# Optimization experiments

Hardware: AMD Instinct MI355X
Metric: run time of the kernel (lower is better)

## Reference

```python
import jax, jax.numpy as jnp
import numpy as np

HIDDEN = 4096
N_HEADS = 32
HEAD_DIM = HIDDEN // N_HEADS
B = 8
S = 1024
N = B * S


def _build_cos_sin(max_pos, head_dim):
    inv_freq = 1.0 / (10000.0 ** (np.arange(0, head_dim, 2, dtype=np.float32) / head_dim))
    t = np.arange(max_pos, dtype=np.float32)
    freqs = np.outer(t, inv_freq)                 # [max_pos, head_dim/2]
    emb = np.concatenate([freqs, freqs], axis=-1)  # [max_pos, head_dim]
    return jnp.asarray(np.cos(emb)), jnp.asarray(np.sin(emb))


def setup_inputs() -> dict:
    key = jax.random.key(0)
    ks = jax.random.split(key, 5)
    cos, sin = _build_cos_sin(S, HEAD_DIM)
    scale = 0.02
    inp = {
        "cos": cos,
        "sin": sin,
        "nz_hidden_states": jax.random.normal(ks[0], (N, HIDDEN), jnp.float32),
        "nz_position_ids": jnp.tile(jnp.arange(S, dtype=jnp.int32), B),
        "cu_seqlens": jnp.arange(B + 1, dtype=jnp.int32) * S,
        "max_seqlen": S,
        "Wq": jax.random.normal(ks[1], (HIDDEN, HIDDEN), jnp.float32) * scale,
        "Wk": jax.random.normal(ks[2], (HIDDEN, HIDDEN), jnp.float32) * scale,
        "Wv": jax.random.normal(ks[3], (HIDDEN, HIDDEN), jnp.float32) * scale,
        "Wo": jax.random.normal(ks[4], (HIDDEN, HIDDEN), jnp.float32) * scale,
    }
    return inp


def _rotate_half(x):
    x1, x2 = jnp.split(x, 2, axis=-1)
    return jnp.concatenate([-x2, x1], axis=-1)


def reference(cos, sin, nz_hidden_states, nz_position_ids, cu_seqlens, max_seqlen, Wq, Wk, Wv, Wo):
    n_tok = nz_hidden_states.shape[0]
    b = cu_seqlens.shape[0] - 1
    s = n_tok // b  # equal-length packing
    h, d = N_HEADS, HEAD_DIM

    q = (nz_hidden_states @ Wq.T).reshape(n_tok, h, d)
    k = (nz_hidden_states @ Wk.T).reshape(n_tok, h, d)
    v = (nz_hidden_states @ Wv.T).reshape(n_tok, h, d)

    # RoPE: cos/sin gathered per token, broadcast over heads
    c = cos[nz_position_ids][:, None, :]  # [N,1,D]
    sn = sin[nz_position_ids][:, None, :]
    q = q * c + _rotate_half(q) * sn
    k = k * c + _rotate_half(k) * sn

    # Varlen causal attention (equal-length segments -> batch reshape)
    qb = q.reshape(b, s, h, d)
    kb = k.reshape(b, s, h, d)
    vb = v.reshape(b, s, h, d)
    scores = jnp.einsum('bqhd,bkhd->bhqk', qb, kb) / jnp.sqrt(jnp.float32(d))
    causal = jnp.tril(jnp.ones((s, s), dtype=bool))
    scores = jnp.where(causal, scores, jnp.finfo(scores.dtype).min)
    probs = jax.nn.softmax(scores, axis=-1)
    out = jnp.einsum('bhqk,bkhd->bqhd', probs, vb).reshape(n_tok, h * d)
    return out @ Wo.T
```

## Files before the change

kernel.cpp:

```cpp
#include <hip/hip_runtime.h>
#include <hip/hip_bf16.h>

#define NTOK 8192
#define HID 4096
#define NHEADS 32
#define HDIM 128
#define SEQ 1024
#define NSTEP (HID / 32)

typedef float f32x4 __attribute__((ext_vector_type(4)));
typedef short bf16x8 __attribute__((ext_vector_type(8)));

__device__ __forceinline__ ushort f2bf(float f) {
  union { float f; unsigned u; } x;
  x.f = f;
  unsigned r = x.u + 0x7fffu + ((x.u >> 16) & 1u);
  return (ushort)(r >> 16);
}
__device__ __forceinline__ float bf2f(ushort h) {
  union { unsigned u; float f; } x;
  x.u = ((unsigned)h) << 16;
  return x.f;
}

__global__ __launch_bounds__(256) void cvt_bf16_kernel(const float4* __restrict__ in,
                                                       ushort4* __restrict__ out, int n4) {
  int i = blockIdx.x * 256 + threadIdx.x;
  if (i < n4) {
    float4 v = in[i];
    ushort4 o;
    o.x = f2bf(v.x); o.y = f2bf(v.y); o.z = f2bf(v.z); o.w = f2bf(v.w);
    out[i] = o;
  }
}


__device__ __forceinline__ void gload16(const void* g, void* l) {
  __builtin_amdgcn_global_load_lds(
      (const __attribute__((address_space(1))) unsigned int*)g,
      (__attribute__((address_space(3))) unsigned int*)l, 16, 0, 0);
}

__device__ __forceinline__ void stage32(const ushort* gA, const ushort* gB,
                                        int rowA0, int rowB0, int k0,
                                        ushort* ldsA, ushort* ldsB, int tid) {
  const int wid = tid >> 6, lane = tid & 63;
#pragma unroll
  for (int q = 0; q < 2; ++q) {
    int wuni = q * 8192 + wid * 1024;
    int off = wuni + lane * 16;
    int row = off >> 6;
    int kb = (off ^ (((row >> 1) & 3) << 4)) & 63;
    gload16(gA + (size_t)(rowA0 + row) * HID + k0 + (kb >> 1), (char*)ldsA + wuni);
    gload16(gB + (size_t)(rowB0 + row) * HID + k0 + (kb >> 1), (char*)ldsB + wuni);
  }
}

#define GSTEP(T, DO_STAGE, VMC)                                                \
  do {                                                                         \
    const char* cA = (const char*)ringA[(T) & 3];                              \
    const char* cB = (const char*)ringB[(T) & 3];                              \
    _Pragma("unroll") for (int ii = 0; ii < 8; ++ii) {                         \
      int L = (wm * 128 + ii * 16 + l15) * 64 + l4 * 16;                       \
      af[ii] = *(const bf16x8*)(cA + (L ^ swzr));                              \
    }                                                                          \
    _Pragma("unroll") for (int jj = 0; jj < 4; ++jj) {                         \
      int L = (wn * 64 + jj * 16 + l15) * 64 + l4 * 16;                        \
      bfr[jj] = *(const bf16x8*)(cB + (L ^ swzr));                             \
    }                                                                          \
    if (DO_STAGE)                                                              \
      stage32(Abf, Bp, m0, n0, ((T) + 3) * 32, ringA[((T) + 3) & 3],           \
              ringB[((T) + 3) & 3], tid);                                      \
    _Pragma("unroll") for (int ii = 0; ii < 8; ++ii)                           \
        _Pragma("unroll") for (int jj = 0; jj < 4; ++jj)                       \
            acc[ii][jj] = __builtin_amdgcn_mfma_f32_16x16x32_bf16(             \
                af[ii], bfr[jj], acc[ii][jj], 0, 0, 0);                        \
    if ((VMC) >= 0) {                                                          \
      asm volatile("s_waitcnt lgkmcnt(0)" ::: "memory");                       \
      if ((VMC) == 4) asm volatile("s_waitcnt vmcnt(4)" ::: "memory");         \
      else asm volatile("s_waitcnt vmcnt(0)" ::: "memory");                    \
      __builtin_amdgcn_s_barrier();                                            \
    }                                                                          \
  } while (0)

template <bool OUTF32>
__global__ __launch_bounds__(512, 2) void gemm256_kernel(
    const ushort* __restrict__ Abf,
    const ushort* __restrict__ B0, const ushort* __restrict__ B1,
    const ushort* __restrict__ B2,
    void* __restrict__ O0, void* __restrict__ O1, void* __restrict__ O2,
    int NTALL) {
  __shared__ __align__(16) ushort ringA[4][8192];
  __shared__ __align__(16) ushort ringB[4][8192];

  const int tid = threadIdx.x;
  const int l = tid & 63, wid = tid >> 6;
  const int wm = wid >> 2, wn = wid & 3;
  const int l15 = l & 15, l4 = l >> 4;
  const int swzr = ((l15 >> 1) & 3) << 4;

  const int nwg = gridDim.x;
  const int cpx = nwg >> 3;
  const int bid = blockIdx.x;
  const int lgid = (bid & 7) * cpx + (bid >> 3);
  const int bandw = NTALL << 3;
  const int band = lgid / bandw, rem = lgid % bandw;
  const int nt = rem >> 3;
  const int mt = (band << 3) + (rem & 7);
  const int m0 = mt * 256;
  const int sel = nt >> 4;
  const int n0 = (nt & 15) * 256;
  const ushort* Bp = (sel == 0) ? B0 : ((sel == 1) ? B1 : B2);
  void* Op = (sel == 0) ? O0 : ((sel == 1) ? O1 : O2);

  f32x4 acc[8][4];
  const f32x4 zero = {0.f, 0.f, 0.f, 0.f};
#pragma unroll
  for (int i = 0; i < 8; ++i)
#pragma unroll
    for (int j = 0; j < 4; ++j) acc[i][j] = zero;

  stage32(Abf, Bp, m0, n0, 0, ringA[0], ringB[0], tid);
  stage32(Abf, Bp, m0, n0, 32, ringA[1], ringB[1], tid);
  stage32(Abf, Bp, m0, n0, 64, ringA[2], ringB[2], tid);
  asm volatile("s_waitcnt vmcnt(4)" ::: "memory");
  __builtin_amdgcn_s_barrier();

  bf16x8 af[8], bfr[4];
  for (int tt = 0; tt < NSTEP - 4; tt += 4) {
    GSTEP(tt + 0, true, 4);
    GSTEP(tt + 1, true, 4);
    GSTEP(tt + 2, true, 4);
    GSTEP(tt + 3, true, 4);
  }
  GSTEP(NSTEP - 4, true, 4);
  GSTEP(NSTEP - 3, false, 0);
  GSTEP(NSTEP - 2, false, -1);
  GSTEP(NSTEP - 1, false, -1);

#pragma unroll
  for (int i = 0; i < 8; ++i) {
    const int row = m0 + wm * 128 + i * 16 + l4 * 4;
#pragma unroll
    for (int j = 0; j < 4; ++j) {
      const int col = n0 + wn * 64 + j * 16 + l15;
#pragma unroll
      for (int r = 0; r < 4; ++r) {
        float v = acc[i][j][r];
        if constexpr (OUTF32)
          ((float*)Op)[(size_t)(row + r) * HID + col] = v;
        else
          ((ushort*)Op)[(size_t)(row + r) * HID + col] = f2bf(v);
      }
    }
  }
}

template <bool ISBF>
__device__ __forceinline__ void stage_tile(ushort* lds, const void* gp, int row0, int k0, int tid) {
  if constexpr (ISBF) {
    const ushort* g = (const ushort*)gp;
#pragma unroll
    for (int i = 0; i < 2; ++i) {
      int row = (tid >> 2) + i * 64;
      int gr = tid & 3;
      bf16x8 v = *(const bf16x8*)(g + (size_t)(row0 + row) * HID + k0 + gr * 8);
      int gs = gr ^ ((row >> 1) & 3);
      *(bf16x8*)((char*)lds + row * 64 + gs * 16) = v;
    }
  } else {
    const float* g = (const float*)gp;
    int row = tid >> 1;
    const float* rp = g + (size_t)(row0 + row) * HID + k0;
#pragma unroll
    for (int i = 0; i < 2; ++i) {
      int gr = (tid & 1) * 2 + i;
      float4 a = *(const float4*)(rp + gr * 8);
      float4 b = *(const float4*)(rp + gr * 8 + 4);
      bf16x8 v;
      v[0] = (short)f2bf(a.x); v[1] = (short)f2bf(a.y);
      v[2] = (short)f2bf(a.z); v[3] = (short)f2bf(a.w);
      v[4] = (short)f2bf(b.x); v[5] = (short)f2bf(b.y);
      v[6] = (short)f2bf(b.z); v[7] = (short)f2bf(b.w);
      int gs = gr ^ ((row >> 1) & 3);
      *(bf16x8*)((char*)lds + row * 64 + gs * 16) = v;
    }
  }
}

template <bool ABF, bool BBF, bool OUTF32>
__global__ __launch_bounds__(256) void gemm_bt_kernel(
    const void* __restrict__ Ap,
    const void* __restrict__ B0, const void* __restrict__ B1, const void* __restrict__ B2,
    void* __restrict__ O0, void* __restrict__ O1, void* __restrict__ O2,
    int ntiles_per_w) {
  __shared__ __align__(16) ushort lA[128 * 32];
  __shared__ __align__(16) ushort lB[128 * 32];
  const int tid = threadIdx.x;
  const int l = tid & 63, wid = tid >> 6;
  const int wm = wid >> 1, wn = wid & 1;
  const int l15 = l & 15, l4 = l >> 4;
  const int mt0 = blockIdx.y * 128;
  const int ntile = blockIdx.x;
  const int sel = ntile / ntiles_per_w;
  const int nt0 = (ntile % ntiles_per_w) * 128;
  const void* Bp = (sel == 0) ? B0 : ((sel == 1) ? B1 : B2);
  void* Op = (sel == 0) ? O0 : ((sel == 1) ? O1 : O2);

  const f32x4 zero = {0.f, 0.f, 0.f, 0.f};
  f32x4 acc[4][4];
#pragma unroll
  for (int i = 0; i < 4; ++i)
#pragma unroll
    for (int j = 0; j < 4; ++j) acc[i][j] = zero;

  for (int k0 = 0; k0 < HID; k0 += 32) {
    stage_tile<ABF>(lA, Ap, mt0, k0, tid);
    stage_tile<BBF>(lB, Bp, nt0, k0, tid);
    __syncthreads();
    bf16x8 af[4], bfr[4];
#pragma unroll
    for (int i = 0; i < 4; ++i) {
      int rowa = wm * 64 + i * 16 + l15;
      int ga = l4 ^ ((rowa >> 1) & 3);
      af[i] = *(const bf16x8*)((const char*)lA + rowa * 64 + ga * 16);
      int rowb = wn * 64 + i * 16 + l15;
      int gb = l4 ^ ((rowb >> 1) & 3);
      bfr[i] = *(const bf16x8*)((const char*)lB + rowb * 64 + gb * 16);
    }
#pragma unroll
    for (int i = 0; i < 4; ++i)
#pragma unroll
      for (int j = 0; j < 4; ++j)
        acc[i][j] = __builtin_amdgcn_mfma_f32_16x16x32_bf16(af[i], bfr[j], acc[i][j], 0, 0, 0);
    __syncthreads();
  }

#pragma unroll
  for (int i = 0; i < 4; ++i) {
#pragma unroll
    for (int j = 0; j < 4; ++j) {
      int row = mt0 + wm * 64 + i * 16 + l4 * 4;
      int col = nt0 + wn * 64 + j * 16 + l15;
#pragma unroll
      for (int r = 0; r < 4; ++r) {
        float v = acc[i][j][r];
        if constexpr (OUTF32)
          ((float*)Op)[(size_t)(row + r) * HID + col] = v;
        else
          ((ushort*)Op)[(size_t)(row + r) * HID + col] = f2bf(v);
      }
    }
  }
}

__global__ __launch_bounds__(256) void rope_kernel(
    ushort* __restrict__ q, ushort* __restrict__ k,
    const float* __restrict__ cosT, const float* __restrict__ sinT,
    const int* __restrict__ pos) {
  int idx = blockIdx.x * 256 + threadIdx.x;
  int token = idx >> 8;
  int head = (idx >> 3) & 31;
  int c = idx & 7;
  int p = pos[token];
  size_t base = (size_t)token * HID + head * HDIM + c * 8;
  bf16x8 ql = *(bf16x8*)(q + base);
  bf16x8 qh = *(bf16x8*)(q + base + 64);
  bf16x8 kl = *(bf16x8*)(k + base);
  bf16x8 kh = *(bf16x8*)(k + base + 64);
  float4 c0 = *(const float4*)(cosT + (size_t)p * HDIM + c * 8);
  float4 c1 = *(const float4*)(cosT + (size_t)p * HDIM + c * 8 + 4);
  float4 s0 = *(const float4*)(sinT + (size_t)p * HDIM + c * 8);
  float4 s1 = *(const float4*)(sinT + (size_t)p * HDIM + c * 8 + 4);
  float cs[8] = {c0.x, c0.y, c0.z, c0.w, c1.x, c1.y, c1.z, c1.w};
  float sn[8] = {s0.x, s0.y, s0.z, s0.w, s1.x, s1.y, s1.z, s1.w};
  const float qsc = 0.08838834764831845f;
  bf16x8 qlo, qho, klo, kho;
#pragma unroll
  for (int j = 0; j < 8; ++j) {
    float qlf = bf2f((ushort)ql[j]), qhf = bf2f((ushort)qh[j]);
    float klf = bf2f((ushort)kl[j]), khf = bf2f((ushort)kh[j]);
    qlo[j] = (short)f2bf((qlf * cs[j] - qhf * sn[j]) * qsc);
    qho[j] = (short)f2bf((qhf * cs[j] + qlf * sn[j]) * qsc);
    klo[j] = (short)f2bf(klf * cs[j] - khf * sn[j]);
    kho[j] = (short)f2bf(khf * cs[j] + klf * sn[j]);
  }
  *(bf16x8*)(q + base) = qlo;
  *(bf16x8*)(q + base + 64) = qho;
  *(bf16x8*)(k + base) = klo;
  *(bf16x8*)(k + base + 64) = kho;
}

#define KVB 64
__global__ __launch_bounds__(512) void attn_kernel(
    const ushort* __restrict__ qb, const ushort* __restrict__ kb,
    const ushort* __restrict__ vb, ushort* __restrict__ ob) {
  __shared__ __align__(16) ushort lK[KVB * 128];
  __shared__ __align__(16) ushort lVT[128 * KVB];
  __shared__ __align__(16) ushort lP[8][16 * KVB];

  const int tid = threadIdx.x;
  const int l = tid & 63, wid = tid >> 6;
  const int l15 = l & 15, l4 = l >> 4;
  const int q0 = (gridDim.x - 1 - blockIdx.x) * 128;
  const int h = blockIdx.y;
  const size_t seqbase = (size_t)blockIdx.z * SEQ;

  bf16x8 qf[4];
  {
    const ushort* qp = qb + (seqbase + q0 + wid * 16 + l15) * HID + h * HDIM + l4 * 8;
#pragma unroll
    for (int kk = 0; kk < 4; ++kk) qf[kk] = *(const bf16x8*)(qp + kk * 32);
  }

  const f32x4 zero = {0.f, 0.f, 0.f, 0.f};
  f32x4 oacc[8];
#pragma unroll
  for (int t = 0; t < 8; ++t) oacc[t] = zero;
  float mrow[4] = {-3e38f, -3e38f, -3e38f, -3e38f};
  float lrow[4] = {0.f, 0.f, 0.f, 0.f};

  const int ntile = q0 / KVB + 2;
  for (int kt = 0; kt < ntile; ++kt) {
    const int k0 = kt * KVB;
    {
      int r = tid >> 3;
      const ushort* kp = kb + (seqbase + k0 + r) * HID + h * HDIM;
#pragma unroll
      for (int i = 0; i < 2; ++i) {
        int g = (tid & 7) * 2 + i;
        bf16x8 kv = *(const bf16x8*)(kp + g * 8);
        int gs = g ^ (r & 7);
        *(bf16x8*)((char*)lK + r * 256 + gs * 16) = kv;
      }
    }
    {
      int d = tid & 127;
      int j0 = (tid >> 7) * 16;
      const ushort* vp = vb + (seqbase + k0 + j0) * HID + h * HDIM + d;
      ushort tmp[16];
#pragma unroll
      for (int j = 0; j < 16; ++j) tmp[j] = vp[(size_t)j * HID];
#pragma unroll
      for (int i = 0; i < 2; ++i) {
        bf16x8 vv;
#pragma unroll
        for (int jj = 0; jj < 8; ++jj) vv[jj] = (short)tmp[i * 8 + jj];
        int g = (j0 >> 3) + i;
        int gs = g ^ (d & 7);
        *(bf16x8*)((char*)lVT + d * 128 + gs * 16) = vv;
      }
    }
    __syncthreads();

    f32x4 s[4];
#pragma unroll
    for (int hf = 0; hf < 4; ++hf) {
      f32x4 c = zero;
      int row = hf * 16 + l15;
#pragma unroll
      for (int kk = 0; kk < 4; ++kk) {
        int gs = (kk * 4 + l4) ^ (row & 7);
        bf16x8 kf = *(const bf16x8*)((const char*)lK + row * 256 + gs * 16);
        c = __builtin_amdgcn_mfma_f32_16x16x32_bf16(qf[kk], kf, c, 0, 0, 0);
      }
      s[hf] = c;
    }

    const int qrow = q0 + wid * 16 + l4 * 4;
#pragma unroll
    for (int r = 0; r < 4; ++r) {
      float sv[4];
#pragma unroll
      for (int hf = 0; hf < 4; ++hf)
        sv[hf] = (k0 + hf * 16 + l15 <= qrow + r) ? s[hf][r] : -1e30f;
      float tmax = fmaxf(fmaxf(sv[0], sv[1]), fmaxf(sv[2], sv[3]));
#pragma unroll
      for (int off = 8; off; off >>= 1) tmax = fmaxf(tmax, __shfl_xor(tmax, off));
      float newm = fmaxf(mrow[r], tmax);
      float sc = __expf(mrow[r] - newm);
      float p[4];
#pragma unroll
      for (int hf = 0; hf < 4; ++hf) p[hf] = __expf(sv[hf] - newm);
      float rs = (p[0] + p[1]) + (p[2] + p[3]);
#pragma unroll
      for (int off = 8; off; off >>= 1) rs += __shfl_xor(rs, off);
      lrow[r] = lrow[r] * sc + rs;
      mrow[r] = newm;
#pragma unroll
      for (int t = 0; t < 8; ++t) oacc[t][r] *= sc;
      int prow = l4 * 4 + r;
      char* pb = (char*)&lP[wid][0] + prow * 128;
#pragma unroll
      for (int hf = 0; hf < 4; ++hf)
        *(ushort*)(pb + (((hf * 16 + l15) * 2) ^ ((prow & 7) << 4))) = f2bf(p[hf]);
    }
    asm volatile("s_waitcnt lgkmcnt(0)" ::: "memory");
    __builtin_amdgcn_sched_barrier(0);

    bf16x8 pf[2];
#pragma unroll
    for (int h2 = 0; h2 < 2; ++h2)
      pf[h2] = *(const bf16x8*)((const char*)&lP[wid][0] + l15 * 128 +
                                (((h2 * 4 + l4) * 16) ^ ((l15 & 7) << 4)));
#pragma unroll
    for (int t = 0; t < 8; ++t) {
      int d = t * 16 + l15;
#pragma unroll
      for (int h2 = 0; h2 < 2; ++h2) {
        int gs = (h2 * 4 + l4) ^ (d & 7);
        bf16x8 vf = *(const bf16x8*)((const char*)lVT + d * 128 + gs * 16);
        oacc[t] = __builtin_amdgcn_mfma_f32_16x16x32_bf16(pf[h2], vf, oacc[t], 0, 0, 0);
      }
    }
    __syncthreads();
  }

#pragma unroll
  for (int r = 0; r < 4; ++r) {
    float inv = 1.0f / lrow[r];
    ushort* op = ob + (seqbase + q0 + wid * 16 + l4 * 4 + r) * HID + h * HDIM + l15;
#pragma unroll
    for (int t = 0; t < 8; ++t) op[t * 16] = f2bf(oacc[t][r] * inv);
  }
}

extern "C" void kernel_launch(void* const* d_in, const int* in_sizes, int n_in,
                              void* d_out, int out_size, void* d_ws, size_t ws_size,
                              hipStream_t stream) {
  const float* cosT = (const float*)d_in[0];
  const float* sinT = (const float*)d_in[1];
  const float* X    = (const float*)d_in[2];
  const int*   pos  = (const int*)d_in[3];
  const float* Wq = (const float*)d_in[6];
  const float* Wk = (const float*)d_in[7];
  const float* Wv = (const float*)d_in[8];
  const float* Wo = (const float*)d_in[9];
  float* out = (float*)d_out;

  char* ws = (char*)d_ws;
  const size_t QKVB = (size_t)NTOK * HID * 2;
  const size_t WB = (size_t)HID * HID * 2;
  const size_t XB = QKVB;
  ushort* qbuf = (ushort*)(ws);
  ushort* kbuf = (ushort*)(ws + QKVB);
  ushort* vbuf = (ushort*)(ws + 2 * QKVB);

  dim3 blk(256);
  const int n4x = NTOK * HID / 4;
  const int n4w = HID * HID / 4;

  const bool fast = ws_size >= 3 * QKVB + XB + 4 * WB;
  const bool mid = !fast && ws_size >= 3 * QKVB + 2 * WB &&
                   (size_t)out_size * 4 >= XB + 2 * WB;

  if (fast || mid) {
    ushort *xb, *wqb, *wkb, *wvb, *wob;
    if (fast) {
      xb  = (ushort*)(ws + 3 * QKVB);
      wqb = (ushort*)(ws + 3 * QKVB + XB);
      wkb = (ushort*)(ws + 3 * QKVB + XB + WB);
      wvb = (ushort*)(ws + 3 * QKVB + XB + 2 * WB);
      wob = (ushort*)(ws + 3 * QKVB + XB + 3 * WB);
    } else {
      xb  = (ushort*)d_out;
      wqb = (ushort*)((char*)d_out + XB);
      wkb = (ushort*)((char*)d_out + XB + WB);
      wvb = (ushort*)(ws + 3 * QKVB);
      wob = (ushort*)(ws + 3 * QKVB + WB);
    }
    cvt_bf16_kernel<<<n4x / 256, blk, 0, stream>>>((const float4*)X, (ushort4*)xb, n4x);
    cvt_bf16_kernel<<<n4w / 256, blk, 0, stream>>>((const float4*)Wq, (ushort4*)wqb, n4w);
    cvt_bf16_kernel<<<n4w / 256, blk, 0, stream>>>((const float4*)Wk, (ushort4*)wkb, n4w);
    cvt_bf16_kernel<<<n4w / 256, blk, 0, stream>>>((const float4*)Wv, (ushort4*)wvb, n4w);
    cvt_bf16_kernel<<<n4w / 256, blk, 0, stream>>>((const float4*)Wo, (ushort4*)wob, n4w);
    gemm256_kernel<false><<<dim3(32 * 48), dim3(512), 0, stream>>>(
        xb, wqb, wkb, wvb, qbuf, kbuf, vbuf, 48);
    rope_kernel<<<NTOK * NHEADS * 8 / 256, blk, 0, stream>>>(qbuf, kbuf, cosT, sinT, pos);
    attn_kernel<<<dim3(8, 32, 8), dim3(512), 0, stream>>>(qbuf, kbuf, vbuf, qbuf);
    gemm256_kernel<true><<<dim3(32 * 16), dim3(512), 0, stream>>>(
        qbuf, wob, wob, wob, out, out, out, 16);
  } else {
    gemm_bt_kernel<false, false, false><<<dim3(96, 64), blk, 0, stream>>>(
        X, Wq, Wk, Wv, qbuf, kbuf, vbuf, 32);
    rope_kernel<<<NTOK * NHEADS * 8 / 256, blk, 0, stream>>>(qbuf, kbuf, cosT, sinT, pos);
    attn_kernel<<<dim3(8, 32, 8), dim3(512), 0, stream>>>(qbuf, kbuf, vbuf, qbuf);
    gemm_bt_kernel<true, false, true><<<dim3(32, 64), blk, 0, stream>>>(
        qbuf, Wo, Wo, Wo, out, out, out, 32);
  }
}
```

Baseline: 1.515 ms.

## Fuse RoPE into QKV GEMM epilogue and register-prefetch K/V tiles in attention

The QKV GEMM now maps each wave's columns so that it holds both halves of every rotate-half pair. This lets the epilogue apply RoPE, plus a query scale factor, directly before storing, which removes the separate rope kernel launch and its read-modify-write pass over Q and K. The attention kernel now prefetches the next K/V tile into registers while computing the current tile, and drops the trailing syncthreads in favour of a barrier at the top of the loop. The costs are extra register pressure and scattered cos/sin/pos loads in the GEMM epilogue.

```diff
diff --git a/kernel.cpp b/kernel.cpp
--- a/kernel.cpp
+++ b/kernel.cpp
@@ -65,7 +65,7 @@
       af[ii] = *(const bf16x8*)(cA + (L ^ swzr));                              \
     }                                                                          \
     _Pragma("unroll") for (int jj = 0; jj < 4; ++jj) {                         \
-      int L = (wn * 64 + jj * 16 + l15) * 64 + l4 * 16;                        \
+      int L = (colbase + (jj & 1) * 16 + (jj >> 1) * 64 + l15) * 64 + l4 * 16; \
       bfr[jj] = *(const bf16x8*)(cB + (L ^ swzr));                             \
     }                                                                          \
     if (DO_STAGE)                                                              \
@@ -83,13 +83,14 @@
     }                                                                          \
   } while (0)
 
-template <bool OUTF32>
+template <bool OUTF32, bool DOROPE>
 __global__ __launch_bounds__(512, 2) void gemm256_kernel(
     const ushort* __restrict__ Abf,
     const ushort* __restrict__ B0, const ushort* __restrict__ B1,
     const ushort* __restrict__ B2,
     void* __restrict__ O0, void* __restrict__ O1, void* __restrict__ O2,
-    int NTALL) {
+    int NTALL, const int* __restrict__ pos,
+    const float* __restrict__ cosT, const float* __restrict__ sinT) {
   __shared__ __align__(16) ushort ringA[4][8192];
   __shared__ __align__(16) ushort ringB[4][8192];
 
@@ -98,6 +99,7 @@
   const int wm = wid >> 2, wn = wid & 3;
   const int l15 = l & 15, l4 = l >> 4;
   const int swzr = ((l15 >> 1) & 3) << 4;
+  const int colbase = (wn >> 1) * 128 + (wn & 1) * 32;
 
   const int nwg = gridDim.x;
   const int cpx = nwg >> 3;
@@ -138,19 +140,41 @@
   GSTEP(NSTEP - 2, false, -1);
   GSTEP(NSTEP - 1, false, -1);
 
-#pragma unroll
-  for (int i = 0; i < 8; ++i) {
-    const int row = m0 + wm * 128 + i * 16 + l4 * 4;
-#pragma unroll
-    for (int j = 0; j < 4; ++j) {
-      const int col = n0 + wn * 64 + j * 16 + l15;
+  if (DOROPE && sel < 2) {
+    const float qsc = (sel == 0) ? 0.08838834764831845f : 1.0f;
+#pragma unroll
+    for (int i = 0; i < 8; ++i) {
 #pragma unroll
       for (int r = 0; r < 4; ++r) {
-        float v = acc[i][j][r];
-        if constexpr (OUTF32)
-          ((float*)Op)[(size_t)(row + r) * HID + col] = v;
-        else
-          ((ushort*)Op)[(size_t)(row + r) * HID + col] = f2bf(v);
+        const int row = m0 + wm * 128 + i * 16 + l4 * 4 + r;
+        const int p = pos[row];
+#pragma unroll
+        for (int jj = 0; jj < 2; ++jj) {
+          const int d = (wn & 1) * 32 + jj * 16 + l15;
+          const float c = cosT[p * HDIM + d];
+          const float s = sinT[p * HDIM + d];
+          const float lo = acc[i][jj][r], hi = acc[i][jj + 2][r];
+          const int col = n0 + colbase + jj * 16 + l15;
+          ((ushort*)Op)[(size_t)row * HID + col] = f2bf((lo * c - hi * s) * qsc);
+          ((ushort*)Op)[(size_t)row * HID + col + 64] = f2bf((hi * c + lo * s) * qsc);
+        }
+      }
+    }
+  } else {
+#pragma unroll
+    for (int i = 0; i < 8; ++i) {
+      const int row = m0 + wm * 128 + i * 16 + l4 * 4;
+#pragma unroll
+      for (int j = 0; j < 4; ++j) {
+        const int col = n0 + colbase + (j & 1) * 16 + (j >> 1) * 64 + l15;
+#pragma unroll
+        for (int r = 0; r < 4; ++r) {
+          float v = acc[i][j][r];
+          if constexpr (OUTF32)
+            ((float*)Op)[(size_t)(row + r) * HID + col] = v;
+          else
+            ((ushort*)Op)[(size_t)(row + r) * HID + col] = f2bf(v);
+        }
       }
     }
   }
@@ -306,6 +330,11 @@
   const int h = blockIdx.y;
   const size_t seqbase = (size_t)blockIdx.z * SEQ;
 
+  const int kr = tid >> 3, kg = (tid & 7) * 2;
+  const int vd = tid & 127, vj0 = (tid >> 7) * 16;
+  const ushort* kgp = kb + (seqbase + kr) * HID + h * HDIM + kg * 8;
+  const ushort* vgp = vb + (seqbase + vj0) * HID + h * HDIM + vd;
+
   bf16x8 qf[4];
   {
     const ushort* qp = qb + (seqbase + q0 + wid * 16 + l15) * HID + h * HDIM + l4 * 8;
@@ -321,34 +350,37 @@
   float lrow[4] = {0.f, 0.f, 0.f, 0.f};
 
   const int ntile = q0 / KVB + 2;
+
+  bf16x8 kreg0 = *(const bf16x8*)(kgp);
+  bf16x8 kreg1 = *(const bf16x8*)(kgp + 8);
+  bf16x8 vreg0, vreg1;
+#pragma unroll
+  for (int j = 0; j < 8; ++j) {
+    vreg0[j] = (short)vgp[(size_t)j * HID];
+    vreg1[j] = (short)vgp[(size_t)(j + 8) * HID];
+  }
+
   for (int kt = 0; kt < ntile; ++kt) {
     const int k0 = kt * KVB;
+    __builtin_amdgcn_s_barrier();
     {
-      int r = tid >> 3;
-      const ushort* kp = kb + (seqbase + k0 + r) * HID + h * HDIM;
-#pragma unroll
-      for (int i = 0; i < 2; ++i) {
-        int g = (tid & 7) * 2 + i;
-        bf16x8 kv = *(const bf16x8*)(kp + g * 8);
-        int gs = g ^ (r & 7);
-        *(bf16x8*)((char*)lK + r * 256 + gs * 16) = kv;
-      }
+      int gs0 = kg ^ (kr & 7), gs1 = (kg + 1) ^ (kr & 7);
+      *(bf16x8*)((char*)lK + kr * 256 + gs0 * 16) = kreg0;
+      *(bf16x8*)((char*)lK + kr * 256 + gs1 * 16) = kreg1;
     }
     {
-      int d = tid & 127;
-      int j0 = (tid >> 7) * 16;
-      const ushort* vp = vb + (seqbase + k0 + j0) * HID + h * HDIM + d;
-      ushort tmp[16];
-#pragma unroll
-      for (int j = 0; j < 16; ++j) tmp[j] = vp[(size_t)j * HID];
-#pragma unroll
-      for (int i = 0; i < 2; ++i) {
-        bf16x8 vv;
-#pragma unroll
-        for (int jj = 0; jj < 8; ++jj) vv[jj] = (short)tmp[i * 8 + jj];
-        int g = (j0 >> 3) + i;
-        int gs = g ^ (d & 7);
-        *(bf16x8*)((char*)lVT + d * 128 + gs * 16) = vv;
+      int g0 = vj0 >> 3;
+      *(bf16x8*)((char*)lVT + vd * 128 + (g0 ^ (vd & 7)) * 16) = vreg0;
+      *(bf16x8*)((char*)lVT + vd * 128 + ((g0 + 1) ^ (vd & 7)) * 16) = vreg1;
+    }
+    if (kt + 1 < ntile) {
+      const size_t off = (size_t)(k0 + KVB) * HID;
+      kreg0 = *(const bf16x8*)(kgp + off);
+      kreg1 = *(const bf16x8*)(kgp + off + 8);
+#pragma unroll
+      for (int j = 0; j < 8; ++j) {
+        vreg0[j] = (short)vgp[off + (size_t)j * HID];
+        vreg1[j] = (short)vgp[off + (size_t)(j + 8) * HID];
       }
     }
     __syncthreads();
@@ -413,7 +445,6 @@
         oacc[t] = __builtin_amdgcn_mfma_f32_16x16x32_bf16(pf[h2], vf, oacc[t], 0, 0, 0);
       }
     }
-    __syncthreads();
   }
 
 #pragma unroll
@@ -474,12 +505,11 @@
     cvt_bf16_kernel<<<n4w / 256, blk, 0, stream>>>((const float4*)Wk, (ushort4*)wkb, n4w);
     cvt_bf16_kernel<<<n4w / 256, blk, 0, stream>>>((const float4*)Wv, (ushort4*)wvb, n4w);
     cvt_bf16_kernel<<<n4w / 256, blk, 0, stream>>>((const float4*)Wo, (ushort4*)wob, n4w);
-    gemm256_kernel<false><<<dim3(32 * 48), dim3(512), 0, stream>>>(
-        xb, wqb, wkb, wvb, qbuf, kbuf, vbuf, 48);
-    rope_kernel<<<NTOK * NHEADS * 8 / 256, blk, 0, stream>>>(qbuf, kbuf, cosT, sinT, pos);
+    gemm256_kernel<false, true><<<dim3(32 * 48), dim3(512), 0, stream>>>(
+        xb, wqb, wkb, wvb, qbuf, kbuf, vbuf, 48, pos, cosT, sinT);
     attn_kernel<<<dim3(8, 32, 8), dim3(512), 0, stream>>>(qbuf, kbuf, vbuf, qbuf);
-    gemm256_kernel<true><<<dim3(32 * 16), dim3(512), 0, stream>>>(
-        qbuf, wob, wob, wob, out, out, out, 16);
+    gemm256_kernel<true, false><<<dim3(32 * 16), dim3(512), 0, stream>>>(
+        qbuf, wob, wob, wob, out, out, out, 16, pos, cosT, sinT);
   } else {
     gemm_bt_kernel<false, false, false><<<dim3(96, 64), blk, 0, stream>>>(
         X, Wq, Wk, Wv, qbuf, kbuf, vbuf, 32);
```

After: 1.483 ms. -2.1%, faster.
